# Kernel tuning notes

Measured on AMD Instinct MI355X. Metric: run time of the kernel, lower is better.

The kernel has to match this reference:

```python
import jax, jax.numpy as jnp
import numpy as np

N = 50000      # nodes
E = 800000     # edges (before self-loops)
F_IN = 256
H = 4          # heads
C1 = 128
C2 = 64
NCLS = 50
NEG_SLOPE = 0.2


def setup_inputs() -> dict:
    key = jax.random.key(0)
    ks = jax.random.split(key, 12)
    x = jax.random.normal(ks[0], (N, F_IN), dtype=jnp.float32)
    edge_index = jax.random.randint(ks[1], (2, E), 0, N, dtype=jnp.int32)
    s1 = 1.0 / np.sqrt(F_IN)
    s2 = 1.0 / np.sqrt(H * C1)
    s3 = 1.0 / np.sqrt(H * C2)
    return {
        "x": x,
        "edge_index": edge_index,
        "W1": jax.random.normal(ks[2], (F_IN, H * C1), dtype=jnp.float32) * s1,
        "a_src1": jax.random.normal(ks[3], (H, C1), dtype=jnp.float32) * s2,
        "a_dst1": jax.random.normal(ks[4], (H, C1), dtype=jnp.float32) * s2,
        "b1": jnp.zeros((H * C1,), dtype=jnp.float32),
        "W2": jax.random.normal(ks[5], (H * C1, H * C2), dtype=jnp.float32) * s2,
        "a_src2": jax.random.normal(ks[6], (H, C2), dtype=jnp.float32) * s3,
        "a_dst2": jax.random.normal(ks[7], (H, C2), dtype=jnp.float32) * s3,
        "b2": jnp.zeros((H * C2,), dtype=jnp.float32),
        "Wf": jax.random.normal(ks[8], (H * C2, NCLS), dtype=jnp.float32) * s3,
        "bf": jnp.zeros((NCLS,), dtype=jnp.float32),
    }


def _gat_conv(x, src, dst, W, a_src, a_dst, b, heads, ch):
    # h: [N, H, C] transformed features
    h = (x @ W).reshape(N, heads, ch)
    # per-node attention halves (standard GAT decomposition, avoids per-edge d-dim gather for scores)
    asrc = jnp.sum(h * a_src[None], axis=-1)  # [N, H]
    adst = jnp.sum(h * a_dst[None], axis=-1)  # [N, H]
    e = jax.nn.leaky_relu(asrc[src] + adst[dst], NEG_SLOPE)  # [E, H]
    # softmax over edges sharing the same destination node
    m = jax.ops.segment_max(e, dst, num_segments=N)          # [N, H]
    ex = jnp.exp(e - m[dst])
    denom = jax.ops.segment_sum(ex, dst, num_segments=N)     # [N, H]
    alpha = ex / (denom[dst] + 1e-16)                        # [E, H]
    msg = h[src] * alpha[:, :, None]                         # [E, H, C]
    out = jax.ops.segment_sum(msg, dst, num_segments=N)      # [N, H, C]
    return out.reshape(N, heads * ch) + b


def reference(x, edge_index, W1, a_src1, a_dst1, b1, W2, a_src2, a_dst2, b2, Wf, bf):
    # PyG GATConv adds self-loops by default
    loops = jnp.arange(N, dtype=edge_index.dtype)
    src = jnp.concatenate([edge_index[0], loops])
    dst = jnp.concatenate([edge_index[1], loops])
    h = _gat_conv(x, src, dst, W1, a_src1, a_dst1, b1, H, C1)
    h = jax.nn.elu(h)
    # F.dropout is identity in eval mode
    h = _gat_conv(h, src, dst, W2, a_src2, a_dst2, b2, H, C2)
    h = jax.nn.elu(h)
    return h @ Wf + bf
```

## Files before the change

kernel.cpp:

```cpp
#include <hip/hip_runtime.h>
#include <hip/hip_bf16.h>
#include <cmath>

#define NN 50000
#define EE 800000
#define ET 850000
#define HH 4
#define CC1 128
#define CC2 64
#define FIN 256
#define NCLS 50

typedef __attribute__((ext_vector_type(8))) short   short8;
typedef __attribute__((ext_vector_type(8))) unsigned short ushort8;
typedef __attribute__((ext_vector_type(4))) unsigned short ushortx4;
typedef __attribute__((ext_vector_type(4))) float   floatx4;

__device__ __forceinline__ unsigned short f2bf(float f) {
    union { float f; unsigned int u; } x; x.f = f;
    unsigned int lsb = (x.u >> 16) & 1u;
    x.u += 0x7fffu + lsb;
    return (unsigned short)(x.u >> 16);
}
__device__ __forceinline__ float bf2f(unsigned short b) {
    union { unsigned int u; float f; } x; x.u = ((unsigned int)b) << 16;
    return x.f;
}

typedef const __attribute__((address_space(1))) unsigned int* glds_gp_t;
typedef __attribute__((address_space(3))) unsigned int* glds_lp_t;
__device__ __forceinline__ void glds16(const void* g, void* l) {
    __builtin_amdgcn_global_load_lds((glds_gp_t)g, (glds_lp_t)l, 16, 0, 0);
}

__global__ __launch_bounds__(256) void cast_bf16(
    const float* __restrict__ in, unsigned short* __restrict__ out, int n4)
{
    int t = blockIdx.x * blockDim.x + threadIdx.x;
    if (t >= n4) return;
    float4 v = *(const float4*)(in + 4 * (size_t)t);
    unsigned short r0 = f2bf(v.x), r1 = f2bf(v.y), r2 = f2bf(v.z), r3 = f2bf(v.w);
    unsigned int lo = (unsigned int)r0 | ((unsigned int)r1 << 16);
    unsigned int hi = (unsigned int)r2 | ((unsigned int)r3 << 16);
    *(uint2*)(out + 4 * (size_t)t) = make_uint2(lo, hi);
}

__global__ __launch_bounds__(256) void transpose_cast(
    const float* __restrict__ W, unsigned short* __restrict__ Wt, int K, int N)
{
    int t = blockIdx.x * blockDim.x + threadIdx.x;
    if (t >= K * N) return;
    int n = t / K, k = t - n * K;
    Wt[t] = f2bf(W[(size_t)k * N + n]);
}

__global__ __launch_bounds__(256) void transpose_cast_pad(
    const float* __restrict__ W, unsigned short* __restrict__ Wt,
    int K, int N, int Npad)
{
    int t = blockIdx.x * blockDim.x + threadIdx.x;
    if (t >= K * Npad) return;
    int n = t / K, k = t - n * K;
    Wt[t] = (n < N) ? f2bf(W[(size_t)k * N + n]) : (unsigned short)0;
}

__global__ __launch_bounds__(256) void gemm_bf16_v2(
    const unsigned short* __restrict__ A,
    const unsigned short* __restrict__ Bt,
    unsigned short* __restrict__ C,
    int M, int N, int K)
{
    __shared__ unsigned short As[128 * 32];
    __shared__ unsigned short Bs[128 * 32];
    int tid = threadIdx.x, wave = tid >> 6, lane = tid & 63;
    int wm = (wave >> 1) * 64, wn = (wave & 1) * 64;
    int row0 = blockIdx.x * 128, col0 = blockIdx.y * 128;
    int lm = lane & 15, lq = lane >> 4, kq = lq * 8;
    floatx4 acc[4][4] = {};

    int srow = wave * 32 + (lane >> 2);
    int skk  = (lane & 3) * 8;
    int gra0 = row0 + srow;      if (gra0 >= M) gra0 = M - 1;
    int gra1 = row0 + srow + 16; if (gra1 >= M) gra1 = M - 1;
    const unsigned short* ga0 = A + (size_t)gra0 * K + skk;
    const unsigned short* ga1 = A + (size_t)gra1 * K + skk;
    const unsigned short* gb0 = Bt + (size_t)(col0 + srow) * K + skk;
    const unsigned short* gb1 = Bt + (size_t)(col0 + srow + 16) * K + skk;
    unsigned short* la0 = &As[(wave * 32) * 32];
    unsigned short* la1 = &As[(wave * 32 + 16) * 32];
    unsigned short* lb0 = &Bs[(wave * 32) * 32];
    unsigned short* lb1 = &Bs[(wave * 32 + 16) * 32];

    for (int k0 = 0; k0 < K; k0 += 32) {
        __syncthreads();
        glds16(ga0 + k0, la0);
        glds16(ga1 + k0, la1);
        glds16(gb0 + k0, lb0);
        glds16(gb1 + k0, lb1);
        __syncthreads();

        short8 af[4], bfr[4];
        #pragma unroll
        for (int mt = 0; mt < 4; ++mt)
            af[mt] = *(const short8*)&As[(wm + mt * 16 + lm) * 32 + kq];
        #pragma unroll
        for (int nt = 0; nt < 4; ++nt)
            bfr[nt] = *(const short8*)&Bs[(wn + nt * 16 + lm) * 32 + kq];
        #pragma unroll
        for (int mt = 0; mt < 4; ++mt)
            #pragma unroll
            for (int nt = 0; nt < 4; ++nt)
                acc[mt][nt] = __builtin_amdgcn_mfma_f32_16x16x32_bf16(
                    af[mt], bfr[nt], acc[mt][nt], 0, 0, 0);
    }

    #pragma unroll
    for (int mt = 0; mt < 4; ++mt) {
        int rbase = row0 + wm + mt * 16 + lq * 4;
        #pragma unroll
        for (int nt = 0; nt < 4; ++nt) {
            int c = col0 + wn + nt * 16 + lm;
            #pragma unroll
            for (int r = 0; r < 4; ++r) {
                int gr = rbase + r;
                if (gr < M) C[(size_t)gr * N + c] = f2bf(acc[mt][nt][r]);
            }
        }
    }
}

__global__ __launch_bounds__(128) void gemm_final(
    const unsigned short* __restrict__ A,
    const unsigned short* __restrict__ Bt,
    const float* __restrict__ bias,
    float* __restrict__ out, int M)
{
    __shared__ unsigned short As[128 * 40];
    __shared__ unsigned short Bs[64 * 40];
    int tid = threadIdx.x, wave = tid >> 6, lane = tid & 63;
    int row0 = blockIdx.x * 128;
    int lm = lane & 15, lq = lane >> 4, kq = lq * 8;
    floatx4 acc[4][4] = {};

    for (int k0 = 0; k0 < 256; k0 += 32) {
        int gr = row0 + tid; if (gr >= M) gr = M - 1;
        const unsigned short* ap = A + (size_t)gr * 256 + k0;
        ushort8 a0 = *(const ushort8*)ap;
        ushort8 a1 = *(const ushort8*)(ap + 8);
        ushort8 a2 = *(const ushort8*)(ap + 16);
        ushort8 a3 = *(const ushort8*)(ap + 24);
        const unsigned short* bp = Bt + (size_t)(tid >> 1) * 256 + k0 + (tid & 1) * 16;
        ushort8 b0 = *(const ushort8*)bp;
        ushort8 b1 = *(const ushort8*)(bp + 8);
        __syncthreads();
        *(ushort8*)&As[tid * 40 + 0]  = a0;
        *(ushort8*)&As[tid * 40 + 8]  = a1;
        *(ushort8*)&As[tid * 40 + 16] = a2;
        *(ushort8*)&As[tid * 40 + 24] = a3;
        *(ushort8*)&Bs[(tid >> 1) * 40 + (tid & 1) * 16]     = b0;
        *(ushort8*)&Bs[(tid >> 1) * 40 + (tid & 1) * 16 + 8] = b1;
        __syncthreads();

        short8 af[4], bfr[4];
        #pragma unroll
        for (int mt = 0; mt < 4; ++mt)
            af[mt] = *(const short8*)&As[(wave * 64 + mt * 16 + lm) * 40 + kq];
        #pragma unroll
        for (int nt = 0; nt < 4; ++nt)
            bfr[nt] = *(const short8*)&Bs[(nt * 16 + lm) * 40 + kq];
        #pragma unroll
        for (int mt = 0; mt < 4; ++mt)
            #pragma unroll
            for (int nt = 0; nt < 4; ++nt)
                acc[mt][nt] = __builtin_amdgcn_mfma_f32_16x16x32_bf16(
                    af[mt], bfr[nt], acc[mt][nt], 0, 0, 0);
    }

    #pragma unroll
    for (int mt = 0; mt < 4; ++mt) {
        int rbase = row0 + wave * 64 + mt * 16 + lq * 4;
        #pragma unroll
        for (int nt = 0; nt < 4; ++nt) {
            int c = nt * 16 + lm;
            if (c >= NCLS) continue;
            float bv = bias[c];
            #pragma unroll
            for (int r = 0; r < 4; ++r) {
                int gr = rbase + r;
                if (gr < M) out[(size_t)gr * NCLS + c] = acc[mt][nt][r] + bv;
            }
        }
    }
}

template<int C>
__global__ __launch_bounds__(256) void attn_scores2(
    const unsigned short* __restrict__ h, const float* __restrict__ a_src,
    const float* __restrict__ a_dst, float* __restrict__ asrc,
    float* __restrict__ adst)
{
    constexpr int HC = HH * C;
    constexpr int CPL = HC / 64;
    int wave = threadIdx.x >> 6;
    int lane = threadIdx.x & 63;
    int n = blockIdx.x * 4 + wave;
    if (n >= NN) return;
    int c0 = lane * CPL;
    int head = c0 / C;
    const unsigned short* hp = h + (size_t)n * HC + c0;
    float hv[CPL];
    if (CPL == 8) {
        ushort8 u = *(const ushort8*)hp;
        #pragma unroll
        for (int c = 0; c < 8; ++c) hv[c] = bf2f(u[c]);
    } else {
        ushortx4 u = *(const ushortx4*)hp;
        #pragma unroll
        for (int c = 0; c < 4; ++c) hv[c] = bf2f(u[c]);
    }
    float s1 = 0.f, s2 = 0.f;
    #pragma unroll
    for (int c = 0; c < CPL; ++c) {
        s1 += hv[c] * a_src[c0 + c];
        s2 += hv[c] * a_dst[c0 + c];
    }
    #pragma unroll
    for (int o = 8; o > 0; o >>= 1) {
        s1 += __shfl_xor(s1, o, 64);
        s2 += __shfl_xor(s2, o, 64);
    }
    if ((lane & 15) == 0) {
        asrc[n * HH + head] = s1;
        adst[n * HH + head] = s2;
    }
}

__global__ void edge_histogram(const int* __restrict__ ei, int* __restrict__ deg)
{
    int t = blockIdx.x * blockDim.x + threadIdx.x;
    if (t >= ET) return;
    int dst = (t < EE) ? ei[EE + t] : (t - EE);
    atomicAdd(&deg[dst], 1);
}

__global__ __launch_bounds__(256) void scan_reduce(
    const int* __restrict__ deg, int* __restrict__ partials)
{
    int i0 = blockIdx.x * 2048 + threadIdx.x * 8;
    int s = 0;
    #pragma unroll
    for (int k = 0; k < 8; ++k) { int i = i0 + k; s += (i < NN) ? deg[i] : 0; }
    #pragma unroll
    for (int o = 32; o > 0; o >>= 1) s += __shfl_xor(s, o, 64);
    __shared__ int ws[4];
    int lane = threadIdx.x & 63, wid = threadIdx.x >> 6;
    if (lane == 0) ws[wid] = s;
    __syncthreads();
    if (threadIdx.x == 0) partials[blockIdx.x] = ws[0] + ws[1] + ws[2] + ws[3];
}

__global__ __launch_bounds__(64) void scan_partials(int* __restrict__ partials, int nb)
{
    int lane = threadIdx.x;
    int v = (lane < nb) ? partials[lane] : 0;
    int s = v;
    #pragma unroll
    for (int o = 1; o < 64; o <<= 1) {
        int t = __shfl_up(s, o, 64);
        if (lane >= o) s += t;
    }
    if (lane < nb) partials[lane] = s - v;
}

__global__ __launch_bounds__(256) void scan_apply(
    const int* __restrict__ deg, const int* __restrict__ partials,
    int* __restrict__ off, int* __restrict__ pos)
{
    int i0 = blockIdx.x * 2048 + threadIdx.x * 8;
    int v[8]; int s = 0;
    #pragma unroll
    for (int k = 0; k < 8; ++k) {
        int i = i0 + k;
        v[k] = (i < NN) ? deg[i] : 0;
        s += v[k];
    }
    int lane = threadIdx.x & 63, wid = threadIdx.x >> 6;
    int sc = s;
    #pragma unroll
    for (int o = 1; o < 64; o <<= 1) {
        int t = __shfl_up(sc, o, 64);
        if (lane >= o) sc += t;
    }
    __shared__ int ws[4];
    if (lane == 63) ws[wid] = sc;
    __syncthreads();
    int woff = partials[blockIdx.x];
    for (int w = 0; w < wid; ++w) woff += ws[w];
    int excl = woff + sc - s;
    #pragma unroll
    for (int k = 0; k < 8; ++k) {
        int i = i0 + k;
        if (i < NN) { off[i] = excl; pos[i] = excl; }
        excl += v[k];
    }
    if (blockIdx.x == 0 && threadIdx.x == 0) off[NN] = ET;
}

__global__ void edge_scatter(const int* __restrict__ ei,
                             int* __restrict__ pos, int* __restrict__ csr_src)
{
    int t = blockIdx.x * blockDim.x + threadIdx.x;
    if (t >= ET) return;
    int src, dst;
    if (t < EE) { src = ei[t]; dst = ei[EE + t]; }
    else        { src = t - EE; dst = t - EE; }
    int p = atomicAdd(&pos[dst], 1);
    csr_src[p] = src;
}

template<int C>
__global__ __launch_bounds__(256) void aggregate5(
    const unsigned short* __restrict__ h, const int* __restrict__ off,
    const int* __restrict__ csr_src, const float* __restrict__ asrc,
    const float* __restrict__ adst, const float* __restrict__ bias,
    unsigned short* __restrict__ outb)
{
    constexpr int HC = HH * C;
    constexpr int LPE = HC / 8;
    constexpr int EPW = 64 / LPE;
    __shared__ float exlds_all[4][64 * HH];
    int wave = threadIdx.x >> 6;
    int lane = threadIdx.x & 63;
    int n = blockIdx.x * 4 + wave;
    if (n >= NN) return;
    float* exlds = exlds_all[wave];
    int el  = (EPW == 1) ? 0 : (lane >> 5);
    int lel = (EPW == 1) ? lane : (lane & 31);
    int coff = lel * 8;
    int hl = coff / C;

    int start = off[n], end = off[n + 1];
    float4 advv = *(const float4*)(adst + (size_t)n * HH);
    float dh0 = 0.f, dh1 = 0.f, dh2 = 0.f, dh3 = 0.f;
    float acc[8] = {0.f, 0.f, 0.f, 0.f, 0.f, 0.f, 0.f, 0.f};

    for (int cb = start; cb < end; cb += 64) {
        int eidx = cb + lane;
        bool valid = eidx < end;
        int s_lane = csr_src[valid ? eidx : end - 1];
        float4 t = *(const float4*)(asrc + (size_t)s_lane * HH);
        float e0 = t.x + advv.x; e0 = e0 > 0.f ? e0 : 0.2f * e0;
        float e1 = t.y + advv.y; e1 = e1 > 0.f ? e1 : 0.2f * e1;
        float e2 = t.z + advv.z; e2 = e2 > 0.f ? e2 : 0.2f * e2;
        float e3 = t.w + advv.w; e3 = e3 > 0.f ? e3 : 0.2f * e3;
        float x0 = valid ? __expf(e0) : 0.f;
        float x1 = valid ? __expf(e1) : 0.f;
        float x2 = valid ? __expf(e2) : 0.f;
        float x3 = valid ? __expf(e3) : 0.f;
        dh0 += x0; dh1 += x1; dh2 += x2; dh3 += x3;
        *(float4*)&exlds[lane * 4] = make_float4(x0, x1, x2, x3);

        int cnt = end - cb; if (cnt > 64) cnt = 64;
        int jmax = (cnt + 4 * EPW - 1) & ~(4 * EPW - 1);
        for (int jj = 0; jj < jmax; jj += 4 * EPW) {
            int sidx[4]; float xs[4]; ushort8 uv[4];
            #pragma unroll
            for (int u = 0; u < 4; ++u) {
                int e_lo = jj + u * EPW;
                if (EPW == 1) {
                    sidx[u] = __builtin_amdgcn_readlane(s_lane, e_lo);
                } else {
                    int sa = __builtin_amdgcn_readlane(s_lane, e_lo);
                    int sb = __builtin_amdgcn_readlane(s_lane, e_lo + 1);
                    sidx[u] = el ? sb : sa;
                }
                xs[u] = exlds[(e_lo + el) * 4 + hl];
                uv[u] = *(const ushort8*)(h + (size_t)sidx[u] * HC + coff);
            }
            #pragma unroll
            for (int u = 0; u < 4; ++u)
                #pragma unroll
                for (int c = 0; c < 8; ++c)
                    acc[c] += xs[u] * bf2f(uv[u][c]);
        }
    }

    #pragma unroll
    for (int o = 32; o > 0; o >>= 1) {
        dh0 += __shfl_xor(dh0, o, 64);
        dh1 += __shfl_xor(dh1, o, 64);
        dh2 += __shfl_xor(dh2, o, 64);
        dh3 += __shfl_xor(dh3, o, 64);
    }
    if (EPW == 2) {
        #pragma unroll
        for (int c = 0; c < 8; ++c)
            acc[c] += __shfl_xor(acc[c], 32, 64);
    }
    float d = (hl == 0) ? dh0 : (hl == 1) ? dh1 : (hl == 2) ? dh2 : dh3;
    float inv = 1.f / (d + 1e-16f);
    if (el == 0) {
        float4 b0 = *(const float4*)(bias + coff);
        float4 b1 = *(const float4*)(bias + coff + 4);
        float bb[8] = {b0.x, b0.y, b0.z, b0.w, b1.x, b1.y, b1.z, b1.w};
        unsigned int pk[4];
        #pragma unroll
        for (int c2 = 0; c2 < 4; ++c2) {
            float ua = acc[2 * c2]     * inv + bb[2 * c2];
            float ub = acc[2 * c2 + 1] * inv + bb[2 * c2 + 1];
            ua = ua > 0.f ? ua : expm1f(ua);
            ub = ub > 0.f ? ub : expm1f(ub);
            pk[c2] = (unsigned int)f2bf(ua) | ((unsigned int)f2bf(ub) << 16);
        }
        *(uint4*)(outb + (size_t)n * HC + coff) = make_uint4(pk[0], pk[1], pk[2], pk[3]);
    }
}

extern "C" void kernel_launch(void* const* d_in, const int* in_sizes, int n_in,
                              void* d_out, int out_size, void* d_ws, size_t ws_size,
                              hipStream_t stream) {
    const float* x      = (const float*)d_in[0];
    const int*   ei     = (const int*)d_in[1];
    const float* W1     = (const float*)d_in[2];
    const float* a_src1 = (const float*)d_in[3];
    const float* a_dst1 = (const float*)d_in[4];
    const float* b1     = (const float*)d_in[5];
    const float* W2     = (const float*)d_in[6];
    const float* a_src2 = (const float*)d_in[7];
    const float* a_dst2 = (const float*)d_in[8];
    const float* b2     = (const float*)d_in[9];
    const float* Wf     = (const float*)d_in[10];
    const float* bf     = (const float*)d_in[11];
    float* out = (float*)d_out;

    char* p = (char*)d_ws;
    unsigned short* xb    = (unsigned short*)p; p += (size_t)NN * FIN * 2;
    unsigned short* h1b   = (unsigned short*)p; p += (size_t)NN * HH * CC1 * 2;
    unsigned short* out1b = (unsigned short*)p; p += (size_t)NN * HH * CC1 * 2;
    unsigned short* h2b   = (unsigned short*)p; p += (size_t)NN * HH * CC2 * 2;
    unsigned short* out2b = (unsigned short*)p; p += (size_t)NN * HH * CC2 * 2;
    unsigned short* W1t   = (unsigned short*)p; p += (size_t)FIN * HH * CC1 * 2;
    unsigned short* W2t   = (unsigned short*)p; p += (size_t)HH * CC1 * HH * CC2 * 2;
    unsigned short* Wft   = (unsigned short*)p; p += (size_t)64 * HH * CC2 * 2;
    float* asrc           = (float*)p;          p += (size_t)NN * HH * 4;
    float* adst           = (float*)p;          p += (size_t)NN * HH * 4;
    int* deg              = (int*)p;            p += (size_t)NN * 4;
    int* csr_off          = (int*)p;            p += (size_t)(NN + 1) * 4 + 12;
    int* csr_pos          = (int*)p;            p += (size_t)NN * 4;
    int* csr_src          = (int*)p;            p += (size_t)ET * 4;
    int* partials         = (int*)p;            p += 64 * 4;

    hipMemsetAsync(deg, 0, NN * sizeof(int), stream);

    cast_bf16<<<(NN * FIN / 4 + 255) / 256, 256, 0, stream>>>(x, xb, NN * FIN / 4);
    transpose_cast<<<(FIN * HH * CC1 + 255) / 256, 256, 0, stream>>>(W1, W1t, FIN, HH * CC1);
    transpose_cast<<<(HH * CC1 * HH * CC2 + 255) / 256, 256, 0, stream>>>(W2, W2t, HH * CC1, HH * CC2);
    transpose_cast_pad<<<(HH * CC2 * 64 + 255) / 256, 256, 0, stream>>>(Wf, Wft, HH * CC2, NCLS, 64);

    const int NB = (NN + 2047) / 2048;
    edge_histogram<<<(ET + 255) / 256, 256, 0, stream>>>(ei, deg);
    scan_reduce<<<NB, 256, 0, stream>>>(deg, partials);
    scan_partials<<<1, 64, 0, stream>>>(partials, NB);
    scan_apply<<<NB, 256, 0, stream>>>(deg, partials, csr_off, csr_pos);
    edge_scatter<<<(ET + 255) / 256, 256, 0, stream>>>(ei, csr_pos, csr_src);

    gemm_bf16_v2<<<dim3((NN + 127) / 128, (HH * CC1) / 128), 256, 0, stream>>>(
        xb, W1t, h1b, NN, HH * CC1, FIN);
    attn_scores2<CC1><<<(NN + 3) / 4, 256, 0, stream>>>(h1b, a_src1, a_dst1, asrc, adst);
    aggregate5<CC1><<<(NN + 3) / 4, 256, 0, stream>>>(h1b, csr_off, csr_src, asrc, adst, b1, out1b);

    gemm_bf16_v2<<<dim3((NN + 127) / 128, (HH * CC2) / 128), 256, 0, stream>>>(
        out1b, W2t, h2b, NN, HH * CC2, HH * CC1);
    attn_scores2<CC2><<<(NN + 3) / 4, 256, 0, stream>>>(h2b, a_src2, a_dst2, asrc, adst);
    aggregate5<CC2><<<(NN + 3) / 4, 256, 0, stream>>>(h2b, csr_off, csr_src, asrc, adst, b2, out2b);

    gemm_final<<<(NN + 127) / 128, 128, 0, stream>>>(out2b, Wft, bf, out, NN);
}
```

Baseline: 512.3 us.

## Precompute per-edge exp scores in a separate kernel and deepen aggregate unroll

Splits the per-edge attention score (gather asrc/adst, leaky-relu, exp) out of the aggregation kernel into a new edge-parallel kernel that writes a float4 per CSR edge. This needs a csr_dst array written during scatter. The aggregation then reads the precomputed exponentials instead of doing a dependent gather and exp inside its latency-bound loop. Separately, the gather unroll goes from 4 to 8 with the feature load issued first, to keep more loads in flight. The split adds an extra kernel launch per layer and about 13.6 MB of extra write-then-read traffic for exf, and the wider unroll raises register pressure.

```diff
diff --git a/kernel.cpp b/kernel.cpp
--- a/kernel.cpp
+++ b/kernel.cpp
@@ -306,8 +306,10 @@
     if (blockIdx.x == 0 && threadIdx.x == 0) off[NN] = ET;
 }
 
-__global__ void edge_scatter(const int* __restrict__ ei,
-                             int* __restrict__ pos, int* __restrict__ csr_src)
+__global__ void edge_scatter2(const int* __restrict__ ei,
+                              int* __restrict__ pos,
+                              int* __restrict__ csr_src,
+                              int* __restrict__ csr_dst)
 {
     int t = blockIdx.x * blockDim.x + threadIdx.x;
     if (t >= ET) return;
@@ -316,18 +318,37 @@
     else        { src = t - EE; dst = t - EE; }
     int p = atomicAdd(&pos[dst], 1);
     csr_src[p] = src;
+    csr_dst[p] = dst;
+}
+
+__global__ __launch_bounds__(256) void edge_scores(
+    const int* __restrict__ csr_src, const int* __restrict__ csr_dst,
+    const float* __restrict__ asrc, const float* __restrict__ adst,
+    float4* __restrict__ exf)
+{
+    int t = blockIdx.x * blockDim.x + threadIdx.x;
+    if (t >= ET) return;
+    int s = csr_src[t];
+    int d = csr_dst[t];
+    float4 a = *(const float4*)(asrc + (size_t)s * HH);
+    float4 b = *(const float4*)(adst + (size_t)d * HH);
+    float e0 = a.x + b.x; e0 = e0 > 0.f ? e0 : 0.2f * e0;
+    float e1 = a.y + b.y; e1 = e1 > 0.f ? e1 : 0.2f * e1;
+    float e2 = a.z + b.z; e2 = e2 > 0.f ? e2 : 0.2f * e2;
+    float e3 = a.w + b.w; e3 = e3 > 0.f ? e3 : 0.2f * e3;
+    exf[t] = make_float4(__expf(e0), __expf(e1), __expf(e2), __expf(e3));
 }
 
 template<int C>
-__global__ __launch_bounds__(256) void aggregate5(
+__global__ __launch_bounds__(256) void aggregate6(
     const unsigned short* __restrict__ h, const int* __restrict__ off,
-    const int* __restrict__ csr_src, const float* __restrict__ asrc,
-    const float* __restrict__ adst, const float* __restrict__ bias,
-    unsigned short* __restrict__ outb)
+    const int* __restrict__ csr_src, const float4* __restrict__ exf,
+    const float* __restrict__ bias, unsigned short* __restrict__ outb)
 {
     constexpr int HC = HH * C;
     constexpr int LPE = HC / 8;
     constexpr int EPW = 64 / LPE;
+    constexpr int UNR = 8;
     __shared__ float exlds_all[4][64 * HH];
     int wave = threadIdx.x >> 6;
     int lane = threadIdx.x & 63;
@@ -340,7 +361,6 @@
     int hl = coff / C;
 
     int start = off[n], end = off[n + 1];
-    float4 advv = *(const float4*)(adst + (size_t)n * HH);
     float dh0 = 0.f, dh1 = 0.f, dh2 = 0.f, dh3 = 0.f;
     float acc[8] = {0.f, 0.f, 0.f, 0.f, 0.f, 0.f, 0.f, 0.f};
 
@@ -348,24 +368,16 @@
         int eidx = cb + lane;
         bool valid = eidx < end;
         int s_lane = csr_src[valid ? eidx : end - 1];
-        float4 t = *(const float4*)(asrc + (size_t)s_lane * HH);
-        float e0 = t.x + advv.x; e0 = e0 > 0.f ? e0 : 0.2f * e0;
-        float e1 = t.y + advv.y; e1 = e1 > 0.f ? e1 : 0.2f * e1;
-        float e2 = t.z + advv.z; e2 = e2 > 0.f ? e2 : 0.2f * e2;
-        float e3 = t.w + advv.w; e3 = e3 > 0.f ? e3 : 0.2f * e3;
-        float x0 = valid ? __expf(e0) : 0.f;
-        float x1 = valid ? __expf(e1) : 0.f;
-        float x2 = valid ? __expf(e2) : 0.f;
-        float x3 = valid ? __expf(e3) : 0.f;
-        dh0 += x0; dh1 += x1; dh2 += x2; dh3 += x3;
-        *(float4*)&exlds[lane * 4] = make_float4(x0, x1, x2, x3);
+        float4 xv = valid ? exf[eidx] : make_float4(0.f, 0.f, 0.f, 0.f);
+        dh0 += xv.x; dh1 += xv.y; dh2 += xv.z; dh3 += xv.w;
+        *(float4*)&exlds[lane * 4] = xv;
 
         int cnt = end - cb; if (cnt > 64) cnt = 64;
-        int jmax = (cnt + 4 * EPW - 1) & ~(4 * EPW - 1);
-        for (int jj = 0; jj < jmax; jj += 4 * EPW) {
-            int sidx[4]; float xs[4]; ushort8 uv[4];
-            #pragma unroll
-            for (int u = 0; u < 4; ++u) {
+        int jmax = (cnt + UNR * EPW - 1) & ~(UNR * EPW - 1);
+        for (int jj = 0; jj < jmax; jj += UNR * EPW) {
+            int sidx[UNR]; float xs[UNR]; ushort8 uv[UNR];
+            #pragma unroll
+            for (int u = 0; u < UNR; ++u) {
                 int e_lo = jj + u * EPW;
                 if (EPW == 1) {
                     sidx[u] = __builtin_amdgcn_readlane(s_lane, e_lo);
@@ -374,11 +386,11 @@
                     int sb = __builtin_amdgcn_readlane(s_lane, e_lo + 1);
                     sidx[u] = el ? sb : sa;
                 }
+                uv[u] = *(const ushort8*)(h + (size_t)sidx[u] * HC + coff);
                 xs[u] = exlds[(e_lo + el) * 4 + hl];
-                uv[u] = *(const ushort8*)(h + (size_t)sidx[u] * HC + coff);
             }
             #pragma unroll
-            for (int u = 0; u < 4; ++u)
+            for (int u = 0; u < UNR; ++u)
                 #pragma unroll
                 for (int c = 0; c < 8; ++c)
                     acc[c] += xs[u] * bf2f(uv[u][c]);
@@ -444,10 +456,12 @@
     unsigned short* Wft   = (unsigned short*)p; p += (size_t)64 * HH * CC2 * 2;
     float* asrc           = (float*)p;          p += (size_t)NN * HH * 4;
     float* adst           = (float*)p;          p += (size_t)NN * HH * 4;
+    float4* exf           = (float4*)p;         p += (size_t)ET * 16;
     int* deg              = (int*)p;            p += (size_t)NN * 4;
     int* csr_off          = (int*)p;            p += (size_t)(NN + 1) * 4 + 12;
     int* csr_pos          = (int*)p;            p += (size_t)NN * 4;
     int* csr_src          = (int*)p;            p += (size_t)ET * 4;
+    int* csr_dst          = (int*)p;            p += (size_t)ET * 4;
     int* partials         = (int*)p;            p += 64 * 4;
 
     hipMemsetAsync(deg, 0, NN * sizeof(int), stream);
@@ -462,17 +476,19 @@
     scan_reduce<<<NB, 256, 0, stream>>>(deg, partials);
     scan_partials<<<1, 64, 0, stream>>>(partials, NB);
     scan_apply<<<NB, 256, 0, stream>>>(deg, partials, csr_off, csr_pos);
-    edge_scatter<<<(ET + 255) / 256, 256, 0, stream>>>(ei, csr_pos, csr_src);
+    edge_scatter2<<<(ET + 255) / 256, 256, 0, stream>>>(ei, csr_pos, csr_src, csr_dst);
 
     gemm_bf16_v2<<<dim3((NN + 127) / 128, (HH * CC1) / 128), 256, 0, stream>>>(
         xb, W1t, h1b, NN, HH * CC1, FIN);
     attn_scores2<CC1><<<(NN + 3) / 4, 256, 0, stream>>>(h1b, a_src1, a_dst1, asrc, adst);
-    aggregate5<CC1><<<(NN + 3) / 4, 256, 0, stream>>>(h1b, csr_off, csr_src, asrc, adst, b1, out1b);
+    edge_scores<<<(ET + 255) / 256, 256, 0, stream>>>(csr_src, csr_dst, asrc, adst, exf);
+    aggregate6<CC1><<<(NN + 3) / 4, 256, 0, stream>>>(h1b, csr_off, csr_src, exf, b1, out1b);
 
     gemm_bf16_v2<<<dim3((NN + 127) / 128, (HH * CC2) / 128), 256, 0, stream>>>(
         out1b, W2t, h2b, NN, HH * CC2, HH * CC1);
     attn_scores2<CC2><<<(NN + 3) / 4, 256, 0, stream>>>(h2b, a_src2, a_dst2, asrc, adst);
-    aggregate5<CC2><<<(NN + 3) / 4, 256, 0, stream>>>(h2b, csr_off, csr_src, asrc, adst, b2, out2b);
+    edge_scores<<<(ET + 255) / 256, 256, 0, stream>>>(csr_src, csr_dst, asrc, adst, exf);
+    aggregate6<CC2><<<(NN + 3) / 4, 256, 0, stream>>>(h2b, csr_off, csr_src, exf, b2, out2b);
 
     gemm_final<<<(NN + 127) / 128, 128, 0, stream>>>(out2b, Wft, bf, out, NN);
 }
```

After: 526.2 us. 2.7% more time.
